# Performance work log

Hardware: AMD Instinct MI355X
Metric: run time of the kernel (lower is better)

Reference implementation:

```python
import jax, jax.numpy as jnp
import numpy as np

N, E = 50000, 800000          # nodes, edges
DC, EC, H, L = 128, 16, 64, 3 # data/edge channels, hidden, num GENConv layers
EPS_MSG = 1e-7                # GENConv message eps
LN_EPS = 1e-5                 # torch LayerNorm eps


def setup_inputs() -> dict:
    key = jax.random.key(0)
    ks = jax.random.split(key, 8)
    s = 0.05
    return {
        "x": jax.random.normal(ks[0], (N, DC), jnp.float32),
        "edge_index": jax.random.randint(ks[1], (2, E), 0, N),
        "edge_attr": jax.random.normal(ks[2], (E, EC), jnp.float32),
        # encoders
        "node_W": jax.random.normal(ks[3], (DC, H), jnp.float32) * s,
        "node_b": jnp.zeros((H,), jnp.float32),
        "edge_W": jax.random.normal(ks[4], (EC, H), jnp.float32) * s,
        "edge_b": jnp.zeros((H,), jnp.float32),
        # per-layer GENConv params (stacked over L layers)
        "t": jnp.ones((L,), jnp.float32),                       # learnable softmax temperature
        "mlp1_W": jax.random.normal(ks[5], (L, H, 2 * H), jnp.float32) * s,
        "mlp1_b": jnp.zeros((L, 2 * H), jnp.float32),
        "mlp_ln_g": jnp.ones((L, 2 * H), jnp.float32),
        "mlp_ln_b": jnp.zeros((L, 2 * H), jnp.float32),
        "mlp2_W": jax.random.normal(ks[6], (L, 2 * H, H), jnp.float32) * s,
        "mlp2_b": jnp.zeros((L, H), jnp.float32),
        # DeepGCNLayer res+ pre-norm params (index 0 also used as the final norm)
        "blk_ln_g": jnp.ones((L, H), jnp.float32),
        "blk_ln_b": jnp.zeros((L, H), jnp.float32),
    }


def _layernorm(h, g, b):
    mu = jnp.mean(h, axis=-1, keepdims=True)
    var = jnp.var(h, axis=-1, keepdims=True)
    return (h - mu) * jax.lax.rsqrt(var + LN_EPS) * g + b


def _genconv(h, src, dst, eattr, t, W1, b1, lng, lnb, W2, b2):
    # message: relu(x_j + edge_attr) + eps   -> [E, H]
    msg = jax.nn.relu(h[src] + eattr) + EPS_MSG
    # softmax aggregation over incoming edges of each dst node (per feature)
    s = msg * t
    smax = jax.ops.segment_max(s, dst, num_segments=N)
    e = jnp.exp(s - smax[dst])
    denom = jax.ops.segment_sum(e, dst, num_segments=N)
    w = e / denom[dst]
    agg = jax.ops.segment_sum(msg * w, dst, num_segments=N)
    out = agg + h  # root (x_r) residual inside GENConv
    # MLP: Linear(H,2H) -> LayerNorm -> ReLU -> Linear(2H,H)
    y = jax.nn.relu(_layernorm(out @ W1 + b1, lng, lnb))
    return y @ W2 + b2


def reference(x, edge_index, edge_attr, node_W, node_b, edge_W, edge_b, t,
              mlp1_W, mlp1_b, mlp_ln_g, mlp_ln_b, mlp2_W, mlp2_b,
              blk_ln_g, blk_ln_b):
    src, dst = edge_index[0], edge_index[1]
    h = x @ node_W + node_b
    ea = edge_attr @ edge_W + edge_b
    # layer 0: conv only (no pre-norm), as in DeeperGCN.forward
    h = _genconv(h, src, dst, ea, t[0], mlp1_W[0], mlp1_b[0],
                 mlp_ln_g[0], mlp_ln_b[0], mlp2_W[0], mlp2_b[0])
    # layers 1..L-1: res+ blocks (norm -> relu -> conv -> residual); dropout=0 in eval
    for i in range(1, L):
        z = jax.nn.relu(_layernorm(h, blk_ln_g[i], blk_ln_b[i]))
        h = h + _genconv(z, src, dst, ea, t[i], mlp1_W[i], mlp1_b[i],
                         mlp_ln_g[i], mlp_ln_b[i], mlp2_W[i], mlp2_b[i])
    # final: layers[0].norm + relu (dropout identity in eval)
    return jax.nn.relu(_layernorm(h, blk_ln_g[0], blk_ln_b[0]))
```

## Files before the change

kernel.cpp:

```cpp
#include <hip/hip_runtime.h>
#include <hip/hip_bf16.h>


#define LN_EPS 1e-5f
#define EPS_MSG 1e-7f

#define PF_NODEB 0
#define PF_EB    64
#define PF_T     128
#define PF_B1    132
#define PF_B2    516
#define PF_LNG   708
#define PF_LNB   1092
#define PF_BG    1476
#define PF_BB    1668
#define PF_TOT   1860
#define PW_NODEWT 0
#define PW_W1T    8192
#define PW_W2T    32768
#define PW_EW     57344
#define PW_EWT    58368
#define PW_TOT    59392

typedef __attribute__((ext_vector_type(8))) __bf16 bf16x8;
typedef __attribute__((ext_vector_type(4))) float floatx4;
typedef __attribute__((ext_vector_type(8))) unsigned short ushort8;

union FragU { bf16x8 v; ushort8 w; unsigned short u[8]; };

__device__ __forceinline__ float b2f(unsigned short u) {
    union { unsigned int i; float f; } v; v.i = ((unsigned int)u) << 16; return v.f;
}
__device__ __forceinline__ unsigned short f2b(float f) {
    unsigned int x = __builtin_bit_cast(unsigned int, f);
    x += 0x7fffu + ((x >> 16) & 1u);
    return (unsigned short)(x >> 16);
}
__device__ __forceinline__ float ldv(const void* p, size_t i, int f32) {
    return f32 ? ((const float*)p)[i] : b2f(((const unsigned short*)p)[i]);
}
__device__ __forceinline__ bf16x8 ld8(const void* p, size_t i, int f32) {
    FragU r;
    if (f32) {
        const float* fp = (const float*)p + i;
        floatx4 a = *(const floatx4*)fp;
        floatx4 b = *(const floatx4*)(fp + 4);
#pragma unroll
        for (int j = 0; j < 4; j++) { r.u[j] = f2b(a[j]); r.u[4 + j] = f2b(b[j]); }
    } else {
        r.w = *(const ushort8*)((const unsigned short*)p + i);
    }
    return r.v;
}
__device__ __forceinline__ int sniff(const void* tptr) {
    return ((const unsigned int*)tptr)[0] == 0x3F800000u ? 1 : 0;
}

__global__ __launch_bounds__(256) void k_wprep(
    const void* __restrict__ nodeW, const void* __restrict__ nodeB,
    const void* __restrict__ eW, const void* __restrict__ eb,
    const void* __restrict__ tp, const void* __restrict__ W1,
    const void* __restrict__ b1, const void* __restrict__ lng,
    const void* __restrict__ lnb, const void* __restrict__ W2,
    const void* __restrict__ b2, const void* __restrict__ bg,
    const void* __restrict__ bbp,
    float* __restrict__ pf, unsigned short* __restrict__ pw,
    int* __restrict__ counts, int N) {
    int f32 = sniff(tp);
    int gid = blockIdx.x * 256 + threadIdx.x;
    if (gid < N) counts[gid] = 0;
    if (gid < 8192) {
        int n = gid >> 7, k = gid & 127;
        pw[gid] = f2b(ldv(nodeW, (size_t)k * 64 + n, f32));
    } else if (gid < 32768) {
        int j = gid - 8192; int i = j >> 13; int r = j & 8191;
        int n = r >> 6, k = r & 63;
        pw[gid] = f2b(ldv(W1, (size_t)i * 8192 + (size_t)k * 128 + n, f32));
    } else if (gid < 57344) {
        int j = gid - 32768; int i = j >> 13; int r = j & 8191;
        int n = r >> 7, k = r & 127;
        pw[gid] = f2b(ldv(W2, (size_t)i * 8192 + (size_t)k * 64 + n, f32));
    } else if (gid < PW_EWT) {
        pw[gid] = f2b(ldv(eW, gid - PW_EW, f32));
    } else if (gid < PW_TOT) {
        int j = gid - PW_EWT; int n = j >> 4, k = j & 15;
        pw[gid] = f2b(ldv(eW, (size_t)k * 64 + n, f32));
    }
    if (gid < PF_TOT) {
        float v; int t = gid;
        if      (t < 64)   v = ldv(nodeB, t, f32);
        else if (t < 128)  v = ldv(eb, t - 64, f32);
        else if (t < 132)  v = (t - 128 < 3) ? ldv(tp, t - 128, f32) : 0.f;
        else if (t < 516)  v = ldv(b1, t - PF_B1, f32);
        else if (t < 708)  v = ldv(b2, t - PF_B2, f32);
        else if (t < 1092) v = ldv(lng, t - PF_LNG, f32);
        else if (t < 1476) v = ldv(lnb, t - PF_LNB, f32);
        else if (t < 1668) v = ldv(bg, t - PF_BG, f32);
        else               v = ldv(bbp, t - PF_BB, f32);
        pf[t] = v;
    }
}

__global__ __launch_bounds__(256) void k_hist_enc(const int* __restrict__ dst,
                                                  int* __restrict__ counts,
                                                  int* __restrict__ rank, int E,
                                                  int hist_blocks,
                                                  const void* __restrict__ x,
                                                  const unsigned short* __restrict__ pw,
                                                  const float* __restrict__ pf,
                                                  unsigned short* __restrict__ zb,
                                                  int N, const void* __restrict__ tptr) {
    __shared__ unsigned short lds[4 * 1088];
    if ((int)blockIdx.x < hist_blocks) {
        int i0 = (blockIdx.x * 256 + threadIdx.x) * 4;
        if (i0 + 4 <= E) {
            int4 d4 = *(const int4*)(dst + i0);
            int r0 = atomicAdd(&counts[d4.x], 1);
            int r1 = atomicAdd(&counts[d4.y], 1);
            int r2 = atomicAdd(&counts[d4.z], 1);
            int r3 = atomicAdd(&counts[d4.w], 1);
            *(int4*)(rank + i0) = make_int4(r0, r1, r2, r3);
        } else {
            for (int i = i0; i < E; i++) rank[i] = atomicAdd(&counts[dst[i]], 1);
        }
        return;
    }
    int f32 = sniff(tptr);
    int bid = blockIdx.x - hist_blocks;
    int wave = threadIdx.x >> 6, lane = threadIdx.x & 63;
    int tm = bid * 4 + wave;
    if (tm >= (N >> 4)) return;
    int l15 = lane & 15, quad = lane >> 4;
    unsigned short* L = lds + wave * 1088;
    int arow = tm * 16 + l15;
    floatx4 acc[4] = {{0,0,0,0},{0,0,0,0},{0,0,0,0},{0,0,0,0}};
#pragma unroll
    for (int kb = 0; kb < 4; kb++) {
        bf16x8 a = ld8(x, (size_t)arow * 128 + kb * 32 + quad * 8, f32);
#pragma unroll
        for (int tn = 0; tn < 4; tn++) {
            FragU b;
            b.w = *(const ushort8*)(pw + PW_NODEWT + (size_t)(tn * 16 + l15) * 128 + kb * 32 + quad * 8);
            acc[tn] = __builtin_amdgcn_mfma_f32_16x16x32_bf16(a, b.v, acc[tn], 0, 0, 0);
        }
    }
#pragma unroll
    for (int tn = 0; tn < 4; tn++) {
        int col = tn * 16 + l15;
        float bv = pf[PF_NODEB + col];
#pragma unroll
        for (int r = 0; r < 4; r++)
            L[(quad * 4 + r) * 68 + col] = f2b(acc[tn][r] + bv);
    }
    __builtin_amdgcn_s_waitcnt(0);
#pragma unroll
    for (int s = 0; s < 2; s++) {
        int row = (lane >> 3) + s * 8;
        int chunk = lane & 7;
        *(ushort8*)(zb + (size_t)(tm * 16 + row) * 64 + chunk * 8) =
            *(const ushort8*)(L + row * 68 + chunk * 8);
    }
}

__global__ __launch_bounds__(256) void k_scan1(const int* __restrict__ counts,
                                               int* __restrict__ bsum, int N) {
    __shared__ int ws[4];
    int tid = threadIdx.x, lane = tid & 63, w = tid >> 6;
    int i0 = blockIdx.x * 1024 + tid * 4;
    int s = 0;
#pragma unroll
    for (int k = 0; k < 4; k++) s += (i0 + k < N) ? counts[i0 + k] : 0;
#pragma unroll
    for (int m = 1; m < 64; m <<= 1) s += __shfl_xor(s, m);
    if (lane == 0) ws[w] = s;
    __syncthreads();
    if (tid == 0) bsum[blockIdx.x] = ws[0] + ws[1] + ws[2] + ws[3];
}

__global__ __launch_bounds__(1024) void k_scan2(const int* __restrict__ bsum,
                                                int* __restrict__ boff, int nb,
                                                int* __restrict__ row_startN) {
    __shared__ int wsum[16];
    int tid = threadIdx.x, lane = tid & 63, w = tid >> 6;
    int v = (tid < nb) ? bsum[tid] : 0;
    int incl = v;
#pragma unroll
    for (int m = 1; m < 64; m <<= 1) { int t = __shfl_up(incl, m); if (lane >= m) incl += t; }
    if (lane == 63) wsum[w] = incl;
    __syncthreads();
    if (w == 0) {
        int s = (lane < 16) ? wsum[lane] : 0;
#pragma unroll
        for (int m = 1; m < 16; m <<= 1) { int t = __shfl_up(s, m); if (lane >= m) s += t; }
        if (lane < 16) wsum[lane] = s;
    }
    __syncthreads();
    int woff = (w > 0) ? wsum[w - 1] : 0;
    if (tid < nb) boff[tid] = woff + incl - v;
    if (tid == nb - 1) row_startN[0] = woff + incl;
}

__global__ __launch_bounds__(256) void k_scan3(const int* __restrict__ counts,
                                               const int* __restrict__ boff,
                                               int* __restrict__ row_start, int N) {
    __shared__ int ws[4];
    int tid = threadIdx.x, lane = tid & 63, w = tid >> 6;
    int i0 = blockIdx.x * 1024 + tid * 4;
    int v[4];
#pragma unroll
    for (int k = 0; k < 4; k++) v[k] = (i0 + k < N) ? counts[i0 + k] : 0;
    int tsum = v[0] + v[1] + v[2] + v[3];
    int incl = tsum;
#pragma unroll
    for (int m = 1; m < 64; m <<= 1) { int t = __shfl_up(incl, m); if (lane >= m) incl += t; }
    if (lane == 63) ws[w] = incl;
    __syncthreads();
    int woff = 0;
    if (w > 0) woff += ws[0];
    if (w > 1) woff += ws[1];
    if (w > 2) woff += ws[2];
    int run = boff[blockIdx.x] + woff + incl - tsum;
#pragma unroll
    for (int k = 0; k < 4; k++) {
        if (i0 + k < N) row_start[i0 + k] = run;
        run += v[k];
    }
}

__global__ __launch_bounds__(256) void k_perm(const int* __restrict__ dst,
                                              const int* __restrict__ src,
                                              const int* __restrict__ rank,
                                              const int* __restrict__ row_start,
                                              int2* __restrict__ sortp, int E) {
    int e0 = (blockIdx.x * 256 + threadIdx.x) * 4;
    if (e0 + 4 <= E) {
        int4 d4 = *(const int4*)(dst + e0);
        int4 r4 = *(const int4*)(rank + e0);
        int4 s4 = *(const int4*)(src + e0);
        int p0 = row_start[d4.x] + r4.x;
        int p1 = row_start[d4.y] + r4.y;
        int p2 = row_start[d4.z] + r4.z;
        int p3 = row_start[d4.w] + r4.w;
        sortp[p0] = make_int2(e0, s4.x);
        sortp[p1] = make_int2(e0 + 1, s4.y);
        sortp[p2] = make_int2(e0 + 2, s4.z);
        sortp[p3] = make_int2(e0 + 3, s4.w);
    } else {
        for (int e = e0; e < E; e++)
            sortp[row_start[dst[e]] + rank[e]] = make_int2(e, src[e]);
    }
}

__global__ __launch_bounds__(256) void k_ea3(const void* __restrict__ eattr,
                                             const int2* __restrict__ sortp,
                                             const unsigned short* __restrict__ pw,
                                             const float* __restrict__ pf,
                                             unsigned short* __restrict__ ea_s,
                                             int E, const void* __restrict__ tptr) {
    __shared__ unsigned short lds[4 * 1088];
    int f32 = sniff(tptr);
    int wave = threadIdx.x >> 6, lane = threadIdx.x & 63;
    int p0 = (blockIdx.x * 4 + wave) * 16;
    if (p0 >= E) return;
    int l15 = lane & 15, quad = lane >> 4;
    unsigned short* L = lds + wave * 1088;
    FragU a;
#pragma unroll
    for (int j = 0; j < 8; j++) a.u[j] = 0;
    if (quad < 2) {
        int p = p0 + l15; if (p >= E) p = E - 1;
        int e = sortp[p].x;
        a.v = ld8(eattr, (size_t)e * 16 + quad * 8, f32);
    }
    floatx4 acc[4] = {{0,0,0,0},{0,0,0,0},{0,0,0,0},{0,0,0,0}};
#pragma unroll
    for (int tn = 0; tn < 4; tn++) {
        FragU b;
#pragma unroll
        for (int j = 0; j < 8; j++) b.u[j] = 0;
        if (quad < 2)
            b.w = *(const ushort8*)(pw + PW_EWT + (size_t)(tn * 16 + l15) * 16 + quad * 8);
        acc[tn] = __builtin_amdgcn_mfma_f32_16x16x32_bf16(a.v, b.v, acc[tn], 0, 0, 0);
    }
#pragma unroll
    for (int tn = 0; tn < 4; tn++) {
        int col = tn * 16 + l15;
        float bv = pf[PF_EB + col];
#pragma unroll
        for (int r = 0; r < 4; r++)
            L[(quad * 4 + r) * 68 + col] = f2b(acc[tn][r] + bv);
    }
    __builtin_amdgcn_s_waitcnt(0);
#pragma unroll
    for (int s = 0; s < 2; s++) {
        int row = (lane >> 3) + s * 8;
        int chunk = lane & 7;
        int grow = p0 + row;
        if (grow < E)
            *(ushort8*)(ea_s + (size_t)grow * 64 + chunk * 8) =
                *(const ushort8*)(L + row * 68 + chunk * 8);
    }
}

__global__ __launch_bounds__(256) void k_copy(const void* __restrict__ eattr,
                                              const int2* __restrict__ sortp,
                                              unsigned short* __restrict__ eattr_s,
                                              int E, const void* __restrict__ tptr) {
    int f32 = sniff(tptr);
    int gid = blockIdx.x * blockDim.x + threadIdx.x;
    int p = gid >> 4;
    int ch = gid & 15;
    if (p >= E) return;
    int e = sortp[p].x;
    float v = ldv(eattr, (size_t)e * 16 + ch, f32);
    eattr_s[(size_t)p * 16 + ch] = f2b(v);
}

__global__ __launch_bounds__(256) void k_edge_seg(const unsigned short* __restrict__ z,
                                                  const int2* __restrict__ sortp,
                                                  const int* __restrict__ row_start,
                                                  const unsigned short* __restrict__ eabuf,
                                                  const float* __restrict__ pf,
                                                  const unsigned short* __restrict__ pw,
                                                  int layer,
                                                  unsigned short* __restrict__ aggz,
                                                  int N, int stream_mode) {
    int wid = (blockIdx.x * blockDim.x + threadIdx.x) >> 6;
    int lane = threadIdx.x & 63;
    if (wid >= N) return;
    float t = pf[PF_T + layer];
    int s0 = row_start[wid], s1 = row_start[wid + 1];
    float num = 0.f, den = 0.f;
    if (stream_mode) {
        int j = s0;
        for (; j + 4 <= s1; j += 4) {
            int sa = sortp[j].y;
            int sb = sortp[j + 1].y;
            int sc = sortp[j + 2].y;
            int sd = sortp[j + 3].y;
            float za = b2f(z[(size_t)sa * 64 + lane]);
            float zb_ = b2f(z[(size_t)sb * 64 + lane]);
            float zc = b2f(z[(size_t)sc * 64 + lane]);
            float zd = b2f(z[(size_t)sd * 64 + lane]);
            float ea = b2f(eabuf[(size_t)j * 64 + lane]);
            float eb = b2f(eabuf[(size_t)(j + 1) * 64 + lane]);
            float ec = b2f(eabuf[(size_t)(j + 2) * 64 + lane]);
            float ed = b2f(eabuf[(size_t)(j + 3) * 64 + lane]);
            float m0 = fmaxf(za + ea, 0.f) + EPS_MSG;
            float m1 = fmaxf(zb_ + eb, 0.f) + EPS_MSG;
            float m2 = fmaxf(zc + ec, 0.f) + EPS_MSG;
            float m3 = fmaxf(zd + ed, 0.f) + EPS_MSG;
            float x0 = __expf(m0 * t);
            float x1 = __expf(m1 * t);
            float x2 = __expf(m2 * t);
            float x3 = __expf(m3 * t);
            num += m0 * x0 + m1 * x1 + m2 * x2 + m3 * x3;
            den += x0 + x1 + x2 + x3;
        }
        for (; j < s1; ++j) {
            int s = sortp[j].y;
            float zv = b2f(z[(size_t)s * 64 + lane]);
            float eav = b2f(eabuf[(size_t)j * 64 + lane]);
            float msg = fmaxf(zv + eav, 0.f) + EPS_MSG;
            float ex = __expf(msg * t);
            num += msg * ex;
            den += ex;
        }
    } else {
        float ew[16];
#pragma unroll
        for (int k = 0; k < 16; k++) ew[k] = b2f(pw[PW_EW + k * 64 + lane]);
        float ebv = pf[PF_EB + lane];
        for (int j = s0; j < s1; ++j) {
            int s = sortp[j].y;
            float zv = b2f(z[(size_t)s * 64 + lane]);
            const unsigned short* ap = eabuf + (size_t)j * 16;
            ushort8 a0 = *(const ushort8*)ap;
            ushort8 a1 = *(const ushort8*)(ap + 8);
            float ea = ebv;
#pragma unroll
            for (int k = 0; k < 8; k++) ea += ew[k] * b2f(a0[k]);
#pragma unroll
            for (int k = 0; k < 8; k++) ea += ew[8 + k] * b2f(a1[k]);
            float msg = fmaxf(zv + ea, 0.f) + EPS_MSG;
            float ex = __expf(msg * t);
            num += msg * ex;
            den += ex;
        }
    }
    float agg = (den > 0.f) ? __fdividef(num, den) : 0.f;
    float root = b2f(z[(size_t)wid * 64 + lane]);
    aggz[(size_t)wid * 64 + lane] = f2b(agg + root);
}

__global__ __launch_bounds__(256) void k_mlp(const unsigned short* __restrict__ aggz,
                                             const unsigned short* __restrict__ pw,
                                             const float* __restrict__ pf,
                                             int layer, float* __restrict__ h,
                                             void* __restrict__ zout,
                                             int N, int res, int last, int zidx,
                                             const void* __restrict__ tptr) {
    __shared__ unsigned short lds[4 * 2176];
    int wave = threadIdx.x >> 6, lane = threadIdx.x & 63;
    int tm = blockIdx.x * 4 + wave;
    if (tm >= (N >> 4)) return;
    int l15 = lane & 15, quad = lane >> 4;
    unsigned short* L = lds + wave * 2176;

    const unsigned short* W1T = pw + PW_W1T + (size_t)layer * 8192;
    int arow = tm * 16 + l15;
    FragU a0, a1;
    a0.w = *(const ushort8*)(aggz + (size_t)arow * 64 + quad * 8);
    a1.w = *(const ushort8*)(aggz + (size_t)arow * 64 + 32 + quad * 8);
    floatx4 acc1[8];
#pragma unroll
    for (int tn = 0; tn < 8; tn++) {
        FragU b0, b1;
        b0.w = *(const ushort8*)(W1T + (size_t)(tn * 16 + l15) * 64 + quad * 8);
        b1.w = *(const ushort8*)(W1T + (size_t)(tn * 16 + l15) * 64 + 32 + quad * 8);
        floatx4 z4 = {0.f, 0.f, 0.f, 0.f};
        z4 = __builtin_amdgcn_mfma_f32_16x16x32_bf16(a0.v, b0.v, z4, 0, 0, 0);
        acc1[tn] = __builtin_amdgcn_mfma_f32_16x16x32_bf16(a1.v, b1.v, z4, 0, 0, 0);
    }
    float s[4] = {0, 0, 0, 0}, q[4] = {0, 0, 0, 0};
#pragma unroll
    for (int tn = 0; tn < 8; tn++) {
        float bv = pf[PF_B1 + layer * 128 + tn * 16 + l15];
#pragma unroll
        for (int r = 0; r < 4; r++) {
            float v = acc1[tn][r] + bv;
            acc1[tn][r] = v;
            s[r] += v; q[r] += v * v;
        }
    }
    float mean[4], rs[4];
#pragma unroll
    for (int r = 0; r < 4; r++) {
        float sr = s[r], qr = q[r];
#pragma unroll
        for (int m = 1; m < 16; m <<= 1) { sr += __shfl_xor(sr, m); qr += __shfl_xor(qr, m); }
        mean[r] = sr * (1.f / 128.f);
        float var = qr * (1.f / 128.f) - mean[r] * mean[r];
        rs[r] = rsqrtf(var + LN_EPS);
    }
#pragma unroll
    for (int tn = 0; tn < 8; tn++) {
        int col = tn * 16 + l15;
        float g = pf[PF_LNG + layer * 128 + col];
        float bb = pf[PF_LNB + layer * 128 + col];
#pragma unroll
        for (int r = 0; r < 4; r++) {
            float y = fmaxf((acc1[tn][r] - mean[r]) * rs[r] * g + bb, 0.f);
            L[(quad * 4 + r) * 136 + col] = f2b(y);
        }
    }
    __builtin_amdgcn_s_waitcnt(0);

    const unsigned short* W2T = pw + PW_W2T + (size_t)layer * 8192;
    floatx4 acc2[4] = {{0,0,0,0},{0,0,0,0},{0,0,0,0},{0,0,0,0}};
#pragma unroll
    for (int kb = 0; kb < 4; kb++) {
        FragU a;
        a.w = *(const ushort8*)(L + l15 * 136 + kb * 32 + quad * 8);
#pragma unroll
        for (int tn = 0; tn < 4; tn++) {
            FragU b;
            b.w = *(const ushort8*)(W2T + (size_t)(tn * 16 + l15) * 128 + kb * 32 + quad * 8);
            acc2[tn] = __builtin_amdgcn_mfma_f32_16x16x32_bf16(a.v, b.v, acc2[tn], 0, 0, 0);
        }
    }
    float v[4][4];
    float s2[4] = {0, 0, 0, 0}, q2[4] = {0, 0, 0, 0};
#pragma unroll
    for (int tn = 0; tn < 4; tn++) {
        int col = tn * 16 + l15;
        float bv = pf[PF_B2 + layer * 64 + col];
#pragma unroll
        for (int r = 0; r < 4; r++) {
            int row = tm * 16 + quad * 4 + r;
            float t = acc2[tn][r] + bv;
            if (res) t += h[(size_t)row * 64 + col];
            v[tn][r] = t;
            s2[r] += t; q2[r] += t * t;
        }
    }
    float* Lf = (float*)L;
    if (!last) {
#pragma unroll
        for (int tn = 0; tn < 4; tn++) {
            int col = tn * 16 + l15;
#pragma unroll
            for (int r = 0; r < 4; r++)
                Lf[(quad * 4 + r) * 68 + col] = v[tn][r];
        }
        __builtin_amdgcn_s_waitcnt(0);
#pragma unroll
        for (int st = 0; st < 4; st++) {
            int row = st * 4 + (lane >> 4);
            int chunk = lane & 15;
            *(floatx4*)(h + (size_t)(tm * 16 + row) * 64 + chunk * 4) =
                *(const floatx4*)(Lf + row * 68 + chunk * 4);
        }
        __builtin_amdgcn_s_waitcnt(0);
    }
    float mean2[4], rs2[4];
#pragma unroll
    for (int r = 0; r < 4; r++) {
        float sr = s2[r], qr = q2[r];
#pragma unroll
        for (int m = 1; m < 16; m <<= 1) { sr += __shfl_xor(sr, m); qr += __shfl_xor(qr, m); }
        mean2[r] = sr * (1.f / 64.f);
        float var = qr * (1.f / 64.f) - mean2[r] * mean2[r];
        rs2[r] = rsqrtf(var + LN_EPS);
    }
    int f32o = last ? sniff(tptr) : 0;
    if (f32o) {
#pragma unroll
        for (int tn = 0; tn < 4; tn++) {
            int col = tn * 16 + l15;
            float g = pf[PF_BG + zidx * 64 + col];
            float bb = pf[PF_BB + zidx * 64 + col];
#pragma unroll
            for (int r = 0; r < 4; r++)
                Lf[(quad * 4 + r) * 68 + col] =
                    fmaxf((v[tn][r] - mean2[r]) * rs2[r] * g + bb, 0.f);
        }
        __builtin_amdgcn_s_waitcnt(0);
#pragma unroll
        for (int st = 0; st < 4; st++) {
            int row = st * 4 + (lane >> 4);
            int chunk = lane & 15;
            *(floatx4*)((float*)zout + (size_t)(tm * 16 + row) * 64 + chunk * 4) =
                *(const floatx4*)(Lf + row * 68 + chunk * 4);
        }
    } else {
#pragma unroll
        for (int tn = 0; tn < 4; tn++) {
            int col = tn * 16 + l15;
            float g = pf[PF_BG + zidx * 64 + col];
            float bb = pf[PF_BB + zidx * 64 + col];
#pragma unroll
            for (int r = 0; r < 4; r++)
                L[(quad * 4 + r) * 68 + col] =
                    f2b(fmaxf((v[tn][r] - mean2[r]) * rs2[r] * g + bb, 0.f));
        }
        __builtin_amdgcn_s_waitcnt(0);
#pragma unroll
        for (int st = 0; st < 2; st++) {
            int row = (lane >> 3) + st * 8;
            int chunk = lane & 7;
            *(ushort8*)((unsigned short*)zout + (size_t)(tm * 16 + row) * 64 + chunk * 8) =
                *(const ushort8*)(L + row * 68 + chunk * 8);
        }
    }
}

extern "C" void kernel_launch(void* const* d_in, const int* in_sizes, int n_in,
                              void* d_out, int out_size, void* d_ws, size_t ws_size,
                              hipStream_t stream) {
    const void* x     = d_in[0];
    const int*  ei    = (const int*)d_in[1];
    const void* eattr = d_in[2];
    const void* nodeW = d_in[3];
    const void* nodeB = d_in[4];
    const void* edgeW = d_in[5];
    const void* edgeB = d_in[6];
    const void* tptr  = d_in[7];
    const void* W1    = d_in[8];
    const void* b1    = d_in[9];
    const void* lng   = d_in[10];
    const void* lnb   = d_in[11];
    const void* W2    = d_in[12];
    const void* b2    = d_in[13];
    const void* bg    = d_in[14];
    const void* bbp   = d_in[15];

    const int N = in_sizes[0] / 128;
    const int E = in_sizes[1] / 2;
    const int* srcp = ei;
    const int* dstp = ei + E;

    auto align256 = [](char* q) { return (char*)(((size_t)q + 255) & ~(size_t)255); };
    char* p = (char*)d_ws;
    float* h   = (float*)p;                    p = align256(p + (size_t)N * 64 * 4);
    unsigned short* zb   = (unsigned short*)p; p = align256(p + (size_t)N * 64 * 2);
    unsigned short* aggz = (unsigned short*)p; p = align256(p + (size_t)N * 64 * 2);
    int* counts     = (int*)p;                 p = align256(p + (size_t)N * 4);
    int* row_start  = (int*)p;                 p = align256(p + (size_t)(N + 1) * 4);
    int* rank       = (int*)p;                 p = align256(p + (size_t)E * 4);
    int nsb = (N + 1023) / 1024;
    int* bsum       = (int*)p;                 p = align256(p + (size_t)nsb * 4);
    int* boff       = (int*)p;                 p = align256(p + (size_t)nsb * 4);
    int2* sortp     = (int2*)p;                p = align256(p + (size_t)E * 8);
    float* pf = (float*)p;                     p = align256(p + (size_t)PF_TOT * 4);
    unsigned short* pw = (unsigned short*)p;   p = align256(p + (size_t)PW_TOT * 2);
    unsigned short* edata = (unsigned short*)p;
    size_t base = (size_t)(p - (char*)d_ws);
    int stream_mode = (ws_size >= base + (size_t)E * 64 * 2) ? 1 : 0;

    auto blocks = [](long waves) { return dim3((unsigned)((waves * 64 + 255) / 256)); };
    int ntm_blocks = (N / 16 + 3) / 4;
    int wprep_blocks = ((N > PW_TOT ? N : PW_TOT) + 255) / 256;
    int hist_blocks = (E + 1023) / 1024;

    k_wprep<<<dim3(wprep_blocks), 256, 0, stream>>>(
        nodeW, nodeB, edgeW, edgeB, tptr, W1, b1, lng, lnb, W2, b2, bg, bbp,
        pf, pw, counts, N);

    k_hist_enc<<<dim3(hist_blocks + ntm_blocks), 256, 0, stream>>>(
        dstp, counts, rank, E, hist_blocks, x, pw, pf, zb, N, tptr);

    k_scan1<<<dim3(nsb), 256, 0, stream>>>(counts, bsum, N);
    k_scan2<<<dim3(1), 1024, 0, stream>>>(bsum, boff, nsb, row_start + N);
    k_scan3<<<dim3(nsb), 256, 0, stream>>>(counts, boff, row_start, N);

    k_perm<<<dim3((E + 1023) / 1024), 256, 0, stream>>>(dstp, srcp, rank,
                                                        row_start, sortp, E);
    if (stream_mode)
        k_ea3<<<dim3(((E + 15) / 16 + 3) / 4), 256, 0, stream>>>(
            eattr, sortp, pw, pf, edata, E, tptr);
    else
        k_copy<<<dim3((E * 16 + 255) / 256), 256, 0, stream>>>(eattr, sortp,
                                                               edata, E, tptr);

    for (int i = 0; i < 3; i++) {
        k_edge_seg<<<blocks(N), 256, 0, stream>>>(zb, sortp, row_start, edata,
                                                  pf, pw, i, aggz, N, stream_mode);
        int last = (i == 2);
        k_mlp<<<dim3(ntm_blocks), 256, 0, stream>>>(
            aggz, pw, pf, i, h, last ? d_out : (void*)zb, N,
            i > 0 ? 1 : 0, last, last ? 0 : (i + 1), tptr);
    }
}
```

Before: 434.9 us.

## Fuse edge softmax aggregation into MLP kernel with ping-pong z buffers

```diff
diff --git a/kernel.cpp b/kernel.cpp
--- a/kernel.cpp
+++ b/kernel.cpp
@@ -316,102 +316,96 @@
     eattr_s[(size_t)p * 16 + ch] = f2b(v);
 }
 
-__global__ __launch_bounds__(256) void k_edge_seg(const unsigned short* __restrict__ z,
-                                                  const int2* __restrict__ sortp,
-                                                  const int* __restrict__ row_start,
-                                                  const unsigned short* __restrict__ eabuf,
-                                                  const float* __restrict__ pf,
-                                                  const unsigned short* __restrict__ pw,
-                                                  int layer,
-                                                  unsigned short* __restrict__ aggz,
-                                                  int N, int stream_mode) {
-    int wid = (blockIdx.x * blockDim.x + threadIdx.x) >> 6;
-    int lane = threadIdx.x & 63;
-    if (wid >= N) return;
-    float t = pf[PF_T + layer];
-    int s0 = row_start[wid], s1 = row_start[wid + 1];
-    float num = 0.f, den = 0.f;
-    if (stream_mode) {
-        int j = s0;
-        for (; j + 4 <= s1; j += 4) {
-            int sa = sortp[j].y;
-            int sb = sortp[j + 1].y;
-            int sc = sortp[j + 2].y;
-            int sd = sortp[j + 3].y;
-            float za = b2f(z[(size_t)sa * 64 + lane]);
-            float zb_ = b2f(z[(size_t)sb * 64 + lane]);
-            float zc = b2f(z[(size_t)sc * 64 + lane]);
-            float zd = b2f(z[(size_t)sd * 64 + lane]);
-            float ea = b2f(eabuf[(size_t)j * 64 + lane]);
-            float eb = b2f(eabuf[(size_t)(j + 1) * 64 + lane]);
-            float ec = b2f(eabuf[(size_t)(j + 2) * 64 + lane]);
-            float ed = b2f(eabuf[(size_t)(j + 3) * 64 + lane]);
-            float m0 = fmaxf(za + ea, 0.f) + EPS_MSG;
-            float m1 = fmaxf(zb_ + eb, 0.f) + EPS_MSG;
-            float m2 = fmaxf(zc + ec, 0.f) + EPS_MSG;
-            float m3 = fmaxf(zd + ed, 0.f) + EPS_MSG;
-            float x0 = __expf(m0 * t);
-            float x1 = __expf(m1 * t);
-            float x2 = __expf(m2 * t);
-            float x3 = __expf(m3 * t);
-            num += m0 * x0 + m1 * x1 + m2 * x2 + m3 * x3;
-            den += x0 + x1 + x2 + x3;
-        }
-        for (; j < s1; ++j) {
-            int s = sortp[j].y;
-            float zv = b2f(z[(size_t)s * 64 + lane]);
-            float eav = b2f(eabuf[(size_t)j * 64 + lane]);
-            float msg = fmaxf(zv + eav, 0.f) + EPS_MSG;
-            float ex = __expf(msg * t);
-            num += msg * ex;
-            den += ex;
-        }
-    } else {
-        float ew[16];
-#pragma unroll
-        for (int k = 0; k < 16; k++) ew[k] = b2f(pw[PW_EW + k * 64 + lane]);
-        float ebv = pf[PF_EB + lane];
-        for (int j = s0; j < s1; ++j) {
-            int s = sortp[j].y;
-            float zv = b2f(z[(size_t)s * 64 + lane]);
-            const unsigned short* ap = eabuf + (size_t)j * 16;
-            ushort8 a0 = *(const ushort8*)ap;
-            ushort8 a1 = *(const ushort8*)(ap + 8);
-            float ea = ebv;
-#pragma unroll
-            for (int k = 0; k < 8; k++) ea += ew[k] * b2f(a0[k]);
-#pragma unroll
-            for (int k = 0; k < 8; k++) ea += ew[8 + k] * b2f(a1[k]);
-            float msg = fmaxf(zv + ea, 0.f) + EPS_MSG;
-            float ex = __expf(msg * t);
-            num += msg * ex;
-            den += ex;
-        }
-    }
-    float agg = (den > 0.f) ? __fdividef(num, den) : 0.f;
-    float root = b2f(z[(size_t)wid * 64 + lane]);
-    aggz[(size_t)wid * 64 + lane] = f2b(agg + root);
-}
-
-__global__ __launch_bounds__(256) void k_mlp(const unsigned short* __restrict__ aggz,
+__global__ __launch_bounds__(256) void k_mlp(const unsigned short* __restrict__ z,
+                                             const int2* __restrict__ sortp,
+                                             const int* __restrict__ row_start,
+                                             const unsigned short* __restrict__ eabuf,
                                              const unsigned short* __restrict__ pw,
                                              const float* __restrict__ pf,
                                              int layer, float* __restrict__ h,
                                              void* __restrict__ zout,
                                              int N, int res, int last, int zidx,
-                                             const void* __restrict__ tptr) {
+                                             const void* __restrict__ tptr,
+                                             int stream_mode) {
     __shared__ unsigned short lds[4 * 2176];
     int wave = threadIdx.x >> 6, lane = threadIdx.x & 63;
     int tm = blockIdx.x * 4 + wave;
     if (tm >= (N >> 4)) return;
     int l15 = lane & 15, quad = lane >> 4;
     unsigned short* L = lds + wave * 2176;
+    float t = pf[PF_T + layer];
+
+    for (int ni = 0; ni < 16; ni++) {
+        int node = tm * 16 + ni;
+        int s0 = row_start[node], s1 = row_start[node + 1];
+        float num = 0.f, den = 0.f;
+        if (stream_mode) {
+            int j = s0;
+            for (; j + 4 <= s1; j += 4) {
+                int sa = sortp[j].y;
+                int sb = sortp[j + 1].y;
+                int sc = sortp[j + 2].y;
+                int sd = sortp[j + 3].y;
+                float za = b2f(z[(size_t)sa * 64 + lane]);
+                float zb_ = b2f(z[(size_t)sb * 64 + lane]);
+                float zc = b2f(z[(size_t)sc * 64 + lane]);
+                float zd = b2f(z[(size_t)sd * 64 + lane]);
+                float ea = b2f(eabuf[(size_t)j * 64 + lane]);
+                float eb = b2f(eabuf[(size_t)(j + 1) * 64 + lane]);
+                float ec = b2f(eabuf[(size_t)(j + 2) * 64 + lane]);
+                float ed = b2f(eabuf[(size_t)(j + 3) * 64 + lane]);
+                float m0 = fmaxf(za + ea, 0.f) + EPS_MSG;
+                float m1 = fmaxf(zb_ + eb, 0.f) + EPS_MSG;
+                float m2 = fmaxf(zc + ec, 0.f) + EPS_MSG;
+                float m3 = fmaxf(zd + ed, 0.f) + EPS_MSG;
+                float x0 = __expf(m0 * t);
+                float x1 = __expf(m1 * t);
+                float x2 = __expf(m2 * t);
+                float x3 = __expf(m3 * t);
+                num += m0 * x0 + m1 * x1 + m2 * x2 + m3 * x3;
+                den += x0 + x1 + x2 + x3;
+            }
+            for (; j < s1; ++j) {
+                int s = sortp[j].y;
+                float zv = b2f(z[(size_t)s * 64 + lane]);
+                float eav = b2f(eabuf[(size_t)j * 64 + lane]);
+                float msg = fmaxf(zv + eav, 0.f) + EPS_MSG;
+                float ex = __expf(msg * t);
+                num += msg * ex;
+                den += ex;
+            }
+        } else {
+            float ew[16];
+#pragma unroll
+            for (int k = 0; k < 16; k++) ew[k] = b2f(pw[PW_EW + k * 64 + lane]);
+            float ebv = pf[PF_EB + lane];
+            for (int j = s0; j < s1; ++j) {
+                int s = sortp[j].y;
+                float zv = b2f(z[(size_t)s * 64 + lane]);
+                const unsigned short* ap = eabuf + (size_t)j * 16;
+                ushort8 a0 = *(const ushort8*)ap;
+                ushort8 a1 = *(const ushort8*)(ap + 8);
+                float ea = ebv;
+#pragma unroll
+                for (int k = 0; k < 8; k++) ea += ew[k] * b2f(a0[k]);
+#pragma unroll
+                for (int k = 0; k < 8; k++) ea += ew[8 + k] * b2f(a1[k]);
+                float msg = fmaxf(zv + ea, 0.f) + EPS_MSG;
+                float ex = __expf(msg * t);
+                num += msg * ex;
+                den += ex;
+            }
+        }
+        float agg = (den > 0.f) ? __fdividef(num, den) : 0.f;
+        float root = b2f(z[(size_t)node * 64 + lane]);
+        L[ni * 68 + lane] = f2b(agg + root);
+    }
+    __builtin_amdgcn_s_waitcnt(0);
 
     const unsigned short* W1T = pw + PW_W1T + (size_t)layer * 8192;
-    int arow = tm * 16 + l15;
     FragU a0, a1;
-    a0.w = *(const ushort8*)(aggz + (size_t)arow * 64 + quad * 8);
-    a1.w = *(const ushort8*)(aggz + (size_t)arow * 64 + 32 + quad * 8);
+    a0.w = *(const ushort8*)(L + l15 * 68 + quad * 8);
+    a1.w = *(const ushort8*)(L + l15 * 68 + 32 + quad * 8);
     floatx4 acc1[8];
 #pragma unroll
     for (int tn = 0; tn < 8; tn++) {
@@ -478,10 +472,10 @@
 #pragma unroll
         for (int r = 0; r < 4; r++) {
             int row = tm * 16 + quad * 4 + r;
-            float t = acc2[tn][r] + bv;
-            if (res) t += h[(size_t)row * 64 + col];
-            v[tn][r] = t;
-            s2[r] += t; q2[r] += t * t;
+            float tt = acc2[tn][r] + bv;
+            if (res) tt += h[(size_t)row * 64 + col];
+            v[tn][r] = tt;
+            s2[r] += tt; q2[r] += tt * tt;
         }
     }
     float* Lf = (float*)L;
@@ -583,8 +577,8 @@
     auto align256 = [](char* q) { return (char*)(((size_t)q + 255) & ~(size_t)255); };
     char* p = (char*)d_ws;
     float* h   = (float*)p;                    p = align256(p + (size_t)N * 64 * 4);
-    unsigned short* zb   = (unsigned short*)p; p = align256(p + (size_t)N * 64 * 2);
-    unsigned short* aggz = (unsigned short*)p; p = align256(p + (size_t)N * 64 * 2);
+    unsigned short* zb0  = (unsigned short*)p; p = align256(p + (size_t)N * 64 * 2);
+    unsigned short* zb1  = (unsigned short*)p; p = align256(p + (size_t)N * 64 * 2);
     int* counts     = (int*)p;                 p = align256(p + (size_t)N * 4);
     int* row_start  = (int*)p;                 p = align256(p + (size_t)(N + 1) * 4);
     int* rank       = (int*)p;                 p = align256(p + (size_t)E * 4);
@@ -598,7 +592,6 @@
     size_t base = (size_t)(p - (char*)d_ws);
     int stream_mode = (ws_size >= base + (size_t)E * 64 * 2) ? 1 : 0;
 
-    auto blocks = [](long waves) { return dim3((unsigned)((waves * 64 + 255) / 256)); };
     int ntm_blocks = (N / 16 + 3) / 4;
     int wprep_blocks = ((N > PW_TOT ? N : PW_TOT) + 255) / 256;
     int hist_blocks = (E + 1023) / 1024;
@@ -608,7 +601,7 @@
         pf, pw, counts, N);
 
     k_hist_enc<<<dim3(hist_blocks + ntm_blocks), 256, 0, stream>>>(
-        dstp, counts, rank, E, hist_blocks, x, pw, pf, zb, N, tptr);
+        dstp, counts, rank, E, hist_blocks, x, pw, pf, zb0, N, tptr);
 
     k_scan1<<<dim3(nsb), 256, 0, stream>>>(counts, bsum, N);
     k_scan2<<<dim3(1), 1024, 0, stream>>>(bsum, boff, nsb, row_start + N);
@@ -623,12 +616,12 @@
         k_copy<<<dim3((E * 16 + 255) / 256), 256, 0, stream>>>(eattr, sortp,
                                                                edata, E, tptr);
 
+    unsigned short* zbufs[2] = {zb0, zb1};
     for (int i = 0; i < 3; i++) {
-        k_edge_seg<<<blocks(N), 256, 0, stream>>>(zb, sortp, row_start, edata,
-                                                  pf, pw, i, aggz, N, stream_mode);
         int last = (i == 2);
         k_mlp<<<dim3(ntm_blocks), 256, 0, stream>>>(
-            aggz, pw, pf, i, h, last ? d_out : (void*)zb, N,
-            i > 0 ? 1 : 0, last, last ? 0 : (i + 1), tptr);
-    }
-}
+            zbufs[i & 1], sortp, row_start, edata, pw, pf, i, h,
+            last ? d_out : (void*)zbufs[(i + 1) & 1], N,
+            i > 0 ? 1 : 0, last, last ? 0 : (i + 1), tptr, stream_mode);
+    }
+}
```

Result: slower. 498.2 us (+14.5%).
